# Kernel optimization log

Hardware: AMD Instinct MI355X
Metric: run time of the kernel (lower is better)

Reference implementation:

```python
import jax, jax.numpy as jnp
import numpy as np

B, S, D_MODEL, N_HEADS, D_K, D_V = 4, 2048, 512, 8, 64, 64
LN_EPS = 1e-5


def setup_inputs() -> dict:
    key = jax.random.key(0)
    ks = jax.random.split(key, 8)
    inp = {
        "input_Q": jax.random.normal(ks[0], (B, S, D_MODEL), dtype=jnp.float32),
        "input_K": jax.random.normal(ks[1], (B, S, D_MODEL), dtype=jnp.float32),
        "input_V": jax.random.normal(ks[2], (B, S, D_MODEL), dtype=jnp.float32),
        "attn_mask": jax.random.randint(ks[3], (B, S, S), 0, 2).astype(jnp.bool_),
        # weights stored [in, out] (torch Linear does x @ W.T; here we use x @ W)
        "W_Q": jax.random.normal(ks[4], (D_MODEL, N_HEADS * D_K), dtype=jnp.float32) * 0.02,
        "W_K": jax.random.normal(ks[5], (D_MODEL, N_HEADS * D_K), dtype=jnp.float32) * 0.02,
        "W_V": jax.random.normal(ks[6], (D_MODEL, N_HEADS * D_V), dtype=jnp.float32) * 0.02,
        "W_O": jax.random.normal(ks[7], (N_HEADS * D_V, D_MODEL), dtype=jnp.float32) * 0.02,
    }
    return inp


def _layernorm(x, eps=LN_EPS):
    mu = jnp.mean(x, axis=-1, keepdims=True)
    var = jnp.mean(jnp.square(x - mu), axis=-1, keepdims=True)
    return (x - mu) * jax.lax.rsqrt(var + eps)


def reference(input_Q, input_K, input_V, attn_mask, W_Q, W_K, W_V, W_O):
    b = input_Q.shape[0]
    # project and split heads: [b, h, s, d]
    Q = (input_Q @ W_Q).reshape(b, -1, N_HEADS, D_K).transpose(0, 2, 1, 3)
    K = (input_K @ W_K).reshape(b, -1, N_HEADS, D_K).transpose(0, 2, 1, 3)
    V = (input_V @ W_V).reshape(b, -1, N_HEADS, D_V).transpose(0, 2, 1, 3)
    scale = 1.0 / np.sqrt(D_K).astype(np.float32)
    # [b, h, s_q, s_k] scores, mask broadcast over heads
    scores = jnp.einsum("bhqd,bhkd->bhqk", Q, K) * scale
    scores = jnp.where(attn_mask[:, None, :, :], jnp.float32(-1e9), scores)
    attn = jax.nn.softmax(scores, axis=-1)
    context = jnp.einsum("bhqk,bhkd->bhqd", attn, V)
    context = context.transpose(0, 2, 1, 3).reshape(b, -1, N_HEADS * D_V)
    output = context @ W_O
    out = _layernorm(output + input_Q)
    return out, attn
```

## Files before the change

### kernel.cpp

```cpp
#include <hip/hip_runtime.h>
#include <hip/hip_bf16.h>
#include <stdint.h>

#define B_  4
#define S_  2048
#define DM  512
#define H_  8
#define DK  64

typedef float        f32x4 __attribute__((ext_vector_type(4)));
typedef short        s16x8 __attribute__((ext_vector_type(8)));
typedef short        s16x4 __attribute__((ext_vector_type(4)));
typedef unsigned int u32x4 __attribute__((ext_vector_type(4)));
typedef unsigned long long u64x4 __attribute__((ext_vector_type(4)));

#define MFMA_B16(a,b,c) __builtin_amdgcn_mfma_f32_16x16x32_bf16(a,b,c,0,0,0)

__device__ __forceinline__ uint32_t bfr(float x) {
  uint32_t u = __float_as_uint(x);
  return (u + 0x7fffu + ((u >> 16) & 1u)) >> 16;
}
__device__ __forceinline__ uint32_t pk2(float a, float b) {
  return ((bfr(b) & 0xffffu) << 16) | (bfr(a) & 0xffffu);
}
__device__ __forceinline__ float uf16(short s) {
  return __uint_as_float(((uint32_t)(uint16_t)s) << 16);
}

__global__ __launch_bounds__(256) void prep_k(const float* __restrict__ w0,
                                              const float* __restrict__ w1,
                                              const float* __restrict__ w2,
                                              const float* __restrict__ w3,
                                              uint16_t* __restrict__ Wt,
                                              const int* __restrict__ mask,
                                              unsigned long long* __restrict__ mbits) {
  __shared__ float Ls[64 * 65];
  const int tid = threadIdx.x;
  if (blockIdx.x < 256) {
    const int bx = blockIdx.x;
    const int z = bx >> 6;
    const int k0 = ((bx >> 3) & 7) * 64, n0 = (bx & 7) * 64;
    const float* W = (z == 0) ? w0 : (z == 1) ? w1 : (z == 2) ? w2 : w3;
    {
      const int r = tid >> 2, c = (tid & 3) * 16;
      const float4* src = (const float4*)(W + (size_t)(k0 + r) * 512 + n0 + c);
      float4 v0 = src[0], v1 = src[1], v2 = src[2], v3 = src[3];
      float* d = Ls + r * 65 + c;
      d[0]=v0.x; d[1]=v0.y; d[2]=v0.z;  d[3]=v0.w;
      d[4]=v1.x; d[5]=v1.y; d[6]=v1.z;  d[7]=v1.w;
      d[8]=v2.x; d[9]=v2.y; d[10]=v2.z; d[11]=v2.w;
      d[12]=v3.x;d[13]=v3.y;d[14]=v3.z; d[15]=v3.w;
    }
    __syncthreads();
    uint16_t* dstbase = Wt + (size_t)z * 262144;
#pragma unroll
    for (int i = 0; i < 2; ++i) {
      int nl = i * 32 + (tid >> 3);
      int kc = (tid & 7) * 8;
      s16x8 v;
#pragma unroll
      for (int jj = 0; jj < 8; ++jj) v[jj] = (short)bfr(Ls[(kc + jj) * 65 + nl]);
      *(s16x8*)(dstbase + (size_t)(n0 + nl) * 512 + k0 + kc) = v;
    }
  } else {
    const int lane = tid & 63;
    const int wid = ((blockIdx.x - 256) * 256 + tid) >> 6;
    for (int w0i = wid * 4; w0i < B_ * S_ * 32; w0i += 8192 * 4) {
      int v0 = __builtin_nontemporal_load(mask + (size_t)(w0i + 0) * 64 + lane);
      int v1 = __builtin_nontemporal_load(mask + (size_t)(w0i + 1) * 64 + lane);
      int v2 = __builtin_nontemporal_load(mask + (size_t)(w0i + 2) * 64 + lane);
      int v3 = __builtin_nontemporal_load(mask + (size_t)(w0i + 3) * 64 + lane);
      unsigned long long b0 = __ballot(v0 != 0), b1 = __ballot(v1 != 0);
      unsigned long long b2 = __ballot(v2 != 0), b3 = __ballot(v3 != 0);
      if (lane == 0) { u64x4 t = {b0, b1, b2, b3}; *(u64x4*)(mbits + w0i) = t; }
    }
  }
}

template <bool PROJ>
__global__ __launch_bounds__(256) void gemm3_k(const float* __restrict__ Xq,
                                               const float* __restrict__ Xk,
                                               const float* __restrict__ Xv,
                                               const uint16_t* __restrict__ Wt,
                                               const uint16_t* __restrict__ Actx,
                                               uint16_t* __restrict__ Qkv,
                                               float* __restrict__ Y) {
  __shared__ __hip_bfloat16 As[128 * 64];
  __shared__ __hip_bfloat16 Bs[128 * 64];
  const int tid = threadIdx.x, lane = tid & 63, w = tid >> 6;
  const int l4 = lane >> 4, lc = lane & 15;
  const int p = blockIdx.x;
  int xm, yn, z;
  if constexpr (PROJ) {
    const int L = (p & 7) * 96 + (p >> 3);
    z = L >> 8; const int r = L & 255; xm = r >> 2; yn = r & 3;
  } else {
    const int L = (p & 7) * 32 + (p >> 3);
    z = 3; xm = L >> 2; yn = L & 3;
  }
  const int m0 = xm * 128, n0 = yn * 128;
  const float* Af = PROJ ? ((z == 0) ? Xq : (z == 1) ? Xk : Xv) : nullptr;
  const uint16_t* Bt = Wt + (size_t)z * 262144;
  const int wm = (w >> 1) * 64, wn = (w & 1) * 64;
  const int srow = tid >> 3;
  const int scol = tid & 7;
  f32x4 acc[4][4] = {};

  float4 raA[4], raB[4]; s16x8 rab[4]; s16x8 rb[4];
  auto loadA = [&](int kk) {
#pragma unroll
    for (int i = 0; i < 4; ++i) {
      int row = i * 32 + srow;
      if constexpr (PROJ) {
        const float4* s = (const float4*)(Af + (size_t)(m0 + row) * 512 + kk + scol * 8);
        raA[i] = s[0]; raB[i] = s[1];
      } else {
        rab[i] = *(const s16x8*)(Actx + (size_t)(m0 + row) * 512 + kk + scol * 8);
      }
    }
  };
  auto loadB = [&](int kk) {
#pragma unroll
    for (int i = 0; i < 4; ++i) {
      int row = i * 32 + srow;
      rb[i] = *(const s16x8*)(Bt + (size_t)(n0 + row) * 512 + kk + scol * 8);
    }
  };
  auto writeAB = [&]() {
#pragma unroll
    for (int i = 0; i < 4; ++i) {
      int row = i * 32 + srow;
      const int c = (scol * 16) ^ ((row & 7) << 4);
      if constexpr (PROJ) {
        u32x4 v;
        v.x = pk2(raA[i].x, raA[i].y); v.y = pk2(raA[i].z, raA[i].w);
        v.z = pk2(raB[i].x, raB[i].y); v.w = pk2(raB[i].z, raB[i].w);
        *(u32x4*)((char*)As + row * 128 + c) = v;
      } else {
        *(s16x8*)((char*)As + row * 128 + c) = rab[i];
      }
      *(s16x8*)((char*)Bs + row * 128 + c) = rb[i];
    }
  };

  loadA(0); loadB(0); writeAB();
  __syncthreads();
  for (int t = 0; t < 8; ++t) {
    if (t < 7) { loadA((t + 1) * 64); loadB((t + 1) * 64); }
    __builtin_amdgcn_s_setprio(1);
#pragma unroll
    for (int kf = 0; kf < 2; ++kf) {
      s16x8 af[4], bg[4];
#pragma unroll
      for (int mf = 0; mf < 4; ++mf) {
        int row = wm + mf * 16 + lc;
        af[mf] = *(const s16x8*)((char*)As + row * 128 +
                                 ((kf * 64 + l4 * 16) ^ ((row & 7) << 4)));
      }
#pragma unroll
      for (int nf = 0; nf < 4; ++nf) {
        int row = wn + nf * 16 + lc;
        bg[nf] = *(const s16x8*)((char*)Bs + row * 128 +
                                 ((kf * 64 + l4 * 16) ^ ((row & 7) << 4)));
      }
#pragma unroll
      for (int mf = 0; mf < 4; ++mf)
#pragma unroll
        for (int nf = 0; nf < 4; ++nf)
          acc[mf][nf] = MFMA_B16(af[mf], bg[nf], acc[mf][nf]);
    }
    __builtin_amdgcn_s_setprio(0);
    if (t < 7) {
      __syncthreads();
      writeAB();
      __syncthreads();
    }
  }
#pragma unroll
  for (int mf = 0; mf < 4; ++mf)
#pragma unroll
    for (int nf = 0; nf < 4; ++nf) {
      int row = m0 + wm + mf * 16 + l4 * 4;
      int col = n0 + wn + nf * 16 + lc;
#pragma unroll
      for (int j = 0; j < 4; ++j) {
        if constexpr (PROJ)
          (Qkv + (size_t)z * 4194304)[(size_t)(row + j) * 512 + col] =
              (uint16_t)bfr(acc[mf][nf][j]);
        else
          Y[(size_t)(row + j) * 512 + col] = acc[mf][nf][j];
      }
    }
}

__global__ __launch_bounds__(256) void attn_k(const uint16_t* __restrict__ Qb,
                                              const uint16_t* __restrict__ Kb,
                                              const uint16_t* __restrict__ Vb,
                                              const unsigned long long* __restrict__ mbits,
                                              float* __restrict__ attn_out,
                                              uint16_t* __restrict__ ctx) {
  __shared__ __hip_bfloat16 Ks[2][64 * 64];
  __shared__ __hip_bfloat16 Vt[64 * 64];
  __shared__ __hip_bfloat16 Ps[4][16 * 72];
  const int tid = threadIdx.x, lane = tid & 63, w = tid >> 6;
  const int l4 = lane >> 4, lc = lane & 15;
  const int p = blockIdx.x;
  const int L = (p & 7) * 128 + (p >> 3);
  const int qt = L & 31, h = (L >> 5) & 7, b = L >> 8;
  const int qbase = qt * 64;
  const int srow = tid >> 3, scol = tid & 7;

  s16x8 aq0, aq1;
  {
    const uint16_t* qp = Qb + ((size_t)(b * S_ + qbase + w * 16 + lc)) * DM + h * DK + l4 * 8;
    aq0 = *(const s16x8*)qp;
    aq1 = *(const s16x8*)(qp + 32);
  }
  const uint16_t* Kbase = Kb + (size_t)(b * S_) * DM + h * DK;
  const uint16_t* Vbase = Vb + (size_t)(b * S_) * DM + h * DK;
  const unsigned long long* mrow = mbits + ((size_t)(b * S_) + qbase + w * 16 + l4 * 4) * 32;

  float lrun[4] = {0.f, 0.f, 0.f, 0.f};
#pragma unroll
  for (int i = 0; i < 2; ++i) {
    int row = i * 32 + srow;
    s16x8 v = *(const s16x8*)(Kbase + (size_t)row * DM + scol * 8);
    *(s16x8*)((char*)Ks[0] + row * 128 + ((scol * 16) ^ ((row & 7) << 4))) = v;
  }
  __syncthreads();
  for (int kt = 0; kt < 32; ++kt) {
    const int cur = kt & 1;
    const int nxt = (kt < 31) ? kt + 1 : kt;
    s16x8 rk0 = *(const s16x8*)(Kbase + (size_t)(nxt * 64 + srow) * DM + scol * 8);
    s16x8 rk1 = *(const s16x8*)(Kbase + (size_t)(nxt * 64 + 32 + srow) * DM + scol * 8);
    unsigned long long mws[4];
#pragma unroll
    for (int j = 0; j < 4; ++j) mws[j] = mrow[j * 32 + kt];
    f32x4 sacc[4] = {};
    __builtin_amdgcn_s_setprio(1);
#pragma unroll
    for (int nf = 0; nf < 4; ++nf) {
      int row = nf * 16 + lc;
#pragma unroll
      for (int kf = 0; kf < 2; ++kf) {
        s16x8 bk = *(const s16x8*)((char*)Ks[cur] + row * 128 +
                                   ((kf * 64 + l4 * 16) ^ ((row & 7) << 4)));
        sacc[nf] = MFMA_B16(kf ? aq1 : aq0, bk, sacc[nf]);
      }
    }
    __builtin_amdgcn_s_setprio(0);
#pragma unroll
    for (int j = 0; j < 4; ++j)
#pragma unroll
      for (int nf = 0; nf < 4; ++nf) {
        float e = __expf(sacc[nf][j] * 0.125f);
        lrun[j] += ((mws[j] >> (nf * 16 + lc)) & 1ull) ? 0.f : e;
      }
    *(s16x8*)((char*)Ks[cur ^ 1] + srow * 128 + ((scol * 16) ^ ((srow & 7) << 4))) = rk0;
    {
      int row = 32 + srow;
      *(s16x8*)((char*)Ks[cur ^ 1] + row * 128 + ((scol * 16) ^ ((row & 7) << 4))) = rk1;
    }
    __syncthreads();
  }
#pragma unroll
  for (int off = 1; off < 16; off <<= 1)
#pragma unroll
    for (int j = 0; j < 4; ++j) lrun[j] += __shfl_xor(lrun[j], off);
  float Li[4];
#pragma unroll
  for (int j = 0; j < 4; ++j) Li[j] = 1.f / lrun[j];

#pragma unroll
  for (int i = 0; i < 2; ++i) {
    int row = i * 32 + srow;
    s16x8 v = *(const s16x8*)(Kbase + (size_t)row * DM + scol * 8);
    *(s16x8*)((char*)Ks[0] + row * 128 + ((scol * 16) ^ ((row & 7) << 4))) = v;
    s16x8 vv = *(const s16x8*)(Vbase + (size_t)row * DM + scol * 8);
#pragma unroll
    for (int jj = 0; jj < 8; ++jj) {
      int d = scol * 8 + jj;
      *(int16_t*)((char*)Vt + ((d * 128 + row * 2) ^ (scol << 4))) = vv[jj];
    }
  }
  __syncthreads();
  f32x4 cacc[4] = {};
  float* arow = attn_out + (((size_t)(b * H_ + h)) * S_ + qbase + w * 16) * S_;
  for (int kt = 0; kt < 32; ++kt) {
    const int cur = kt & 1;
    const int nxt = (kt < 31) ? kt + 1 : kt;
    s16x8 rk0 = *(const s16x8*)(Kbase + (size_t)(nxt * 64 + srow) * DM + scol * 8);
    s16x8 rk1 = *(const s16x8*)(Kbase + (size_t)(nxt * 64 + 32 + srow) * DM + scol * 8);
    s16x8 rv0 = *(const s16x8*)(Vbase + (size_t)(nxt * 64 + srow) * DM + scol * 8);
    s16x8 rv1 = *(const s16x8*)(Vbase + (size_t)(nxt * 64 + 32 + srow) * DM + scol * 8);
    unsigned long long mws[4];
#pragma unroll
    for (int j = 0; j < 4; ++j) mws[j] = mrow[j * 32 + kt];
    f32x4 sacc[4] = {};
    __builtin_amdgcn_s_setprio(1);
#pragma unroll
    for (int nf = 0; nf < 4; ++nf) {
      int row = nf * 16 + lc;
#pragma unroll
      for (int kf = 0; kf < 2; ++kf) {
        s16x8 bk = *(const s16x8*)((char*)Ks[cur] + row * 128 +
                                   ((kf * 64 + l4 * 16) ^ ((row & 7) << 4)));
        sacc[nf] = MFMA_B16(kf ? aq1 : aq0, bk, sacc[nf]);
      }
    }
    __builtin_amdgcn_s_setprio(0);
#pragma unroll
    for (int j = 0; j < 4; ++j)
#pragma unroll
      for (int nf = 0; nf < 4; ++nf) {
        float e = __expf(sacc[nf][j] * 0.125f);
        float p2 = ((mws[j] >> (nf * 16 + lc)) & 1ull) ? 0.f : e * Li[j];
        *(uint16_t*)((char*)Ps[w] + (l4 * 4 + j) * 144 + (nf * 16 + lc) * 2) = (uint16_t)bfr(p2);
      }
    s16x8 ap0 = *(const s16x8*)((char*)Ps[w] + lc * 144 + l4 * 16);
    s16x8 ap1 = *(const s16x8*)((char*)Ps[w] + lc * 144 + 64 + l4 * 16);
#pragma unroll
    for (int j = 0; j < 4; ++j) {
      const int r = j * 4 + (lane >> 4);
      s16x4 pv = *(const s16x4*)((char*)Ps[w] + r * 144 + (lane & 15) * 8);
      f32x4 o;
      o[0] = uf16(pv[0]); o[1] = uf16(pv[1]); o[2] = uf16(pv[2]); o[3] = uf16(pv[3]);
      __builtin_nontemporal_store(o,
          (f32x4*)(arow + (size_t)r * S_ + kt * 64 + (lane & 15) * 4));
    }
    __builtin_amdgcn_s_setprio(1);
#pragma unroll
    for (int nf = 0; nf < 4; ++nf) {
      int d = nf * 16 + lc;
#pragma unroll
      for (int kf = 0; kf < 2; ++kf) {
        s16x8 bv = *(const s16x8*)((char*)Vt +
                     ((d * 128 + kf * 64 + l4 * 16) ^ ((((d >> 3)) & 7) << 4)));
        cacc[nf] = MFMA_B16(kf ? ap1 : ap0, bv, cacc[nf]);
      }
    }
    __builtin_amdgcn_s_setprio(0);
    __syncthreads();
    *(s16x8*)((char*)Ks[cur ^ 1] + srow * 128 + ((scol * 16) ^ ((srow & 7) << 4))) = rk0;
    {
      int row = 32 + srow;
      *(s16x8*)((char*)Ks[cur ^ 1] + row * 128 + ((scol * 16) ^ ((row & 7) << 4))) = rk1;
    }
#pragma unroll
    for (int jj = 0; jj < 8; ++jj) {
      int d = scol * 8 + jj;
      *(int16_t*)((char*)Vt + ((d * 128 + srow * 2) ^ (scol << 4))) = rv0[jj];
      *(int16_t*)((char*)Vt + ((d * 128 + (32 + srow) * 2) ^ (scol << 4))) = rv1[jj];
    }
    __syncthreads();
  }
#pragma unroll
  for (int nf = 0; nf < 4; ++nf) {
    int d = nf * 16 + lc;
#pragma unroll
    for (int j = 0; j < 4; ++j) {
      int q = qbase + w * 16 + l4 * 4 + j;
      ctx[((size_t)(b * S_ + q)) * DM + h * DK + d] = (uint16_t)bfr(cacc[nf][j]);
    }
  }
}

__global__ __launch_bounds__(256) void ln_k(const float* __restrict__ Y,
                                            const float* __restrict__ X,
                                            float* __restrict__ out) {
  const int lane = threadIdx.x & 63, w = threadIdx.x >> 6;
  const size_t row = (size_t)blockIdx.x * 4 + w;
  const float4* y = (const float4*)(Y + row * 512);
  const float4* x = (const float4*)(X + row * 512);
  float4 a0 = y[lane * 2], a1 = y[lane * 2 + 1];
  float4 b0 = x[lane * 2], b1 = x[lane * 2 + 1];
  float v[8] = {a0.x + b0.x, a0.y + b0.y, a0.z + b0.z, a0.w + b0.w,
                a1.x + b1.x, a1.y + b1.y, a1.z + b1.z, a1.w + b1.w};
  float s = 0.f, ss = 0.f;
#pragma unroll
  for (int j = 0; j < 8; ++j) { s += v[j]; ss += v[j] * v[j]; }
#pragma unroll
  for (int off = 1; off < 64; off <<= 1) {
    s += __shfl_xor(s, off);
    ss += __shfl_xor(ss, off);
  }
  float mean = s * (1.f / 512.f);
  float var = ss * (1.f / 512.f) - mean * mean;
  float rstd = rsqrtf(var + 1e-5f);
  float4 o0 = make_float4((v[0] - mean) * rstd, (v[1] - mean) * rstd,
                          (v[2] - mean) * rstd, (v[3] - mean) * rstd);
  float4 o1 = make_float4((v[4] - mean) * rstd, (v[5] - mean) * rstd,
                          (v[6] - mean) * rstd, (v[7] - mean) * rstd);
  float4* o = (float4*)(out + row * 512);
  o[lane * 2] = o0;
  o[lane * 2 + 1] = o1;
}

extern "C" void kernel_launch(void* const* d_in, const int* in_sizes, int n_in,
                              void* d_out, int out_size, void* d_ws, size_t ws_size,
                              hipStream_t stream) {
  const float* Xq = (const float*)d_in[0];
  const float* Xk = (const float*)d_in[1];
  const float* Xv = (const float*)d_in[2];
  const int*   mask = (const int*)d_in[3];
  const float* Wq = (const float*)d_in[4];
  const float* Wk = (const float*)d_in[5];
  const float* Wv = (const float*)d_in[6];
  const float* Wo = (const float*)d_in[7];

  float* out  = (float*)d_out;
  float* attn = out + (size_t)B_ * S_ * DM;

  char* ws = (char*)d_ws;
  uint16_t* Qb = (uint16_t*)(ws);
  uint16_t* Kb = (uint16_t*)(ws + (8u  << 20));
  uint16_t* Vb = (uint16_t*)(ws + (16u << 20));
  uint16_t* Cx = (uint16_t*)(ws + (24u << 20));
  float*    Y  = (float*)   (ws + (32u << 20));
  uint16_t* Wt = (uint16_t*)(ws + (48u << 20));
  unsigned long long* mb = (unsigned long long*)(ws + (50u << 20));

  prep_k<<<2304, 256, 0, stream>>>(Wq, Wk, Wv, Wo, Wt, mask, mb);

  gemm3_k<true><<<768, 256, 0, stream>>>(Xq, Xk, Xv, Wt, nullptr, Qb, nullptr);

  attn_k<<<1024, 256, 0, stream>>>(Qb, Kb, Vb, mb, attn, Cx);

  gemm3_k<false><<<256, 256, 0, stream>>>(nullptr, nullptr, nullptr, Wt, Cx, nullptr, Y);
  ln_k<<<2048, 256, 0, stream>>>(Y, Xq, out);
}
```

Before: 226.6 us.

## Load K fragments directly from global memory and double-buffer V in LDS

The attention kernel stops staging K tiles through shared memory. Each wave now reads its K MFMA operands straight from global memory (cached) in both the row-sum pass and the output pass, which removes the K LDS writes and the per-iteration barrier in the first pass. The V transpose buffer becomes double-buffered, so one of the two barriers per iteration in the second pass can go. The trade is that K reads are now 16-byte per-lane gathers across rows with a 1 KB stride, served from L1/L2 instead of LDS, and their latency is exposed right before the MFMAs.

```diff
diff --git a/kernel.cpp b/kernel.cpp
--- a/kernel.cpp
+++ b/kernel.cpp
@@ -199,8 +199,7 @@
                                               const unsigned long long* __restrict__ mbits,
                                               float* __restrict__ attn_out,
                                               uint16_t* __restrict__ ctx) {
-  __shared__ __hip_bfloat16 Ks[2][64 * 64];
-  __shared__ __hip_bfloat16 Vt[64 * 64];
+  __shared__ __hip_bfloat16 Vt[2][64 * 64];
   __shared__ __hip_bfloat16 Ps[4][16 * 72];
   const int tid = threadIdx.x, lane = tid & 63, w = tid >> 6;
   const int l4 = lane >> 4, lc = lane & 15;
@@ -221,18 +220,7 @@
   const unsigned long long* mrow = mbits + ((size_t)(b * S_) + qbase + w * 16 + l4 * 4) * 32;
 
   float lrun[4] = {0.f, 0.f, 0.f, 0.f};
-#pragma unroll
-  for (int i = 0; i < 2; ++i) {
-    int row = i * 32 + srow;
-    s16x8 v = *(const s16x8*)(Kbase + (size_t)row * DM + scol * 8);
-    *(s16x8*)((char*)Ks[0] + row * 128 + ((scol * 16) ^ ((row & 7) << 4))) = v;
-  }
-  __syncthreads();
   for (int kt = 0; kt < 32; ++kt) {
-    const int cur = kt & 1;
-    const int nxt = (kt < 31) ? kt + 1 : kt;
-    s16x8 rk0 = *(const s16x8*)(Kbase + (size_t)(nxt * 64 + srow) * DM + scol * 8);
-    s16x8 rk1 = *(const s16x8*)(Kbase + (size_t)(nxt * 64 + 32 + srow) * DM + scol * 8);
     unsigned long long mws[4];
 #pragma unroll
     for (int j = 0; j < 4; ++j) mws[j] = mrow[j * 32 + kt];
@@ -240,11 +228,10 @@
     __builtin_amdgcn_s_setprio(1);
 #pragma unroll
     for (int nf = 0; nf < 4; ++nf) {
-      int row = nf * 16 + lc;
 #pragma unroll
       for (int kf = 0; kf < 2; ++kf) {
-        s16x8 bk = *(const s16x8*)((char*)Ks[cur] + row * 128 +
-                                   ((kf * 64 + l4 * 16) ^ ((row & 7) << 4)));
+        s16x8 bk = *(const s16x8*)(Kbase +
+            (size_t)(kt * 64 + nf * 16 + lc) * DM + kf * 32 + l4 * 8);
         sacc[nf] = MFMA_B16(kf ? aq1 : aq0, bk, sacc[nf]);
       }
     }
@@ -256,12 +243,6 @@
         float e = __expf(sacc[nf][j] * 0.125f);
         lrun[j] += ((mws[j] >> (nf * 16 + lc)) & 1ull) ? 0.f : e;
       }
-    *(s16x8*)((char*)Ks[cur ^ 1] + srow * 128 + ((scol * 16) ^ ((srow & 7) << 4))) = rk0;
-    {
-      int row = 32 + srow;
-      *(s16x8*)((char*)Ks[cur ^ 1] + row * 128 + ((scol * 16) ^ ((row & 7) << 4))) = rk1;
-    }
-    __syncthreads();
   }
 #pragma unroll
   for (int off = 1; off < 16; off <<= 1)
@@ -274,13 +255,11 @@
 #pragma unroll
   for (int i = 0; i < 2; ++i) {
     int row = i * 32 + srow;
-    s16x8 v = *(const s16x8*)(Kbase + (size_t)row * DM + scol * 8);
-    *(s16x8*)((char*)Ks[0] + row * 128 + ((scol * 16) ^ ((row & 7) << 4))) = v;
     s16x8 vv = *(const s16x8*)(Vbase + (size_t)row * DM + scol * 8);
 #pragma unroll
     for (int jj = 0; jj < 8; ++jj) {
       int d = scol * 8 + jj;
-      *(int16_t*)((char*)Vt + ((d * 128 + row * 2) ^ (scol << 4))) = vv[jj];
+      *(int16_t*)((char*)Vt[0] + ((d * 128 + row * 2) ^ (scol << 4))) = vv[jj];
     }
   }
   __syncthreads();
@@ -288,11 +267,11 @@
   float* arow = attn_out + (((size_t)(b * H_ + h)) * S_ + qbase + w * 16) * S_;
   for (int kt = 0; kt < 32; ++kt) {
     const int cur = kt & 1;
-    const int nxt = (kt < 31) ? kt + 1 : kt;
-    s16x8 rk0 = *(const s16x8*)(Kbase + (size_t)(nxt * 64 + srow) * DM + scol * 8);
-    s16x8 rk1 = *(const s16x8*)(Kbase + (size_t)(nxt * 64 + 32 + srow) * DM + scol * 8);
-    s16x8 rv0 = *(const s16x8*)(Vbase + (size_t)(nxt * 64 + srow) * DM + scol * 8);
-    s16x8 rv1 = *(const s16x8*)(Vbase + (size_t)(nxt * 64 + 32 + srow) * DM + scol * 8);
+    s16x8 rv0, rv1;
+    if (kt < 31) {
+      rv0 = *(const s16x8*)(Vbase + (size_t)((kt + 1) * 64 + srow) * DM + scol * 8);
+      rv1 = *(const s16x8*)(Vbase + (size_t)((kt + 1) * 64 + 32 + srow) * DM + scol * 8);
+    }
     unsigned long long mws[4];
 #pragma unroll
     for (int j = 0; j < 4; ++j) mws[j] = mrow[j * 32 + kt];
@@ -300,11 +279,10 @@
     __builtin_amdgcn_s_setprio(1);
 #pragma unroll
     for (int nf = 0; nf < 4; ++nf) {
-      int row = nf * 16 + lc;
 #pragma unroll
       for (int kf = 0; kf < 2; ++kf) {
-        s16x8 bk = *(const s16x8*)((char*)Ks[cur] + row * 128 +
-                                   ((kf * 64 + l4 * 16) ^ ((row & 7) << 4)));
+        s16x8 bk = *(const s16x8*)(Kbase +
+            (size_t)(kt * 64 + nf * 16 + lc) * DM + kf * 32 + l4 * 8);
         sacc[nf] = MFMA_B16(kf ? aq1 : aq0, bk, sacc[nf]);
       }
     }
@@ -334,23 +312,19 @@
       int d = nf * 16 + lc;
 #pragma unroll
       for (int kf = 0; kf < 2; ++kf) {
-        s16x8 bv = *(const s16x8*)((char*)Vt +
+        s16x8 bv = *(const s16x8*)((char*)Vt[cur] +
                      ((d * 128 + kf * 64 + l4 * 16) ^ ((((d >> 3)) & 7) << 4)));
         cacc[nf] = MFMA_B16(kf ? ap1 : ap0, bv, cacc[nf]);
       }
     }
     __builtin_amdgcn_s_setprio(0);
-    __syncthreads();
-    *(s16x8*)((char*)Ks[cur ^ 1] + srow * 128 + ((scol * 16) ^ ((srow & 7) << 4))) = rk0;
-    {
-      int row = 32 + srow;
-      *(s16x8*)((char*)Ks[cur ^ 1] + row * 128 + ((scol * 16) ^ ((row & 7) << 4))) = rk1;
-    }
-#pragma unroll
-    for (int jj = 0; jj < 8; ++jj) {
-      int d = scol * 8 + jj;
-      *(int16_t*)((char*)Vt + ((d * 128 + srow * 2) ^ (scol << 4))) = rv0[jj];
-      *(int16_t*)((char*)Vt + ((d * 128 + (32 + srow) * 2) ^ (scol << 4))) = rv1[jj];
+    if (kt < 31) {
+#pragma unroll
+      for (int jj = 0; jj < 8; ++jj) {
+        int d = scol * 8 + jj;
+        *(int16_t*)((char*)Vt[cur ^ 1] + ((d * 128 + srow * 2) ^ (scol << 4))) = rv0[jj];
+        *(int16_t*)((char*)Vt[cur ^ 1] + ((d * 128 + (32 + srow) * 2) ^ (scol << 4))) = rv1[jj];
+      }
     }
     __syncthreads();
   }
```

Result: slower. 451.1 us (+99.0%).
